# Performance work log

Measured on AMD Instinct MI355X. Metric: run time of the kernel, lower is better.

## Reference

```python
import jax, jax.numpy as jnp
import numpy as np

H = 256  # hidden_size
B = 8192  # batch
S = 1024  # seq_length


def setup_inputs() -> dict:
    key = jax.random.key(0)
    ks = jax.random.split(key, 12)
    lim_g = 1.0 / np.sqrt(1 + H)  # torch Linear default init bound, fan_in = 1+H
    lim_o = 1.0 / np.sqrt(H)
    def lin(k, out_dim, in_dim, lim):
        kw, kb = jax.random.split(k)
        W = jax.random.uniform(kw, (out_dim, in_dim), jnp.float32, -lim, lim)
        b = jax.random.uniform(kb, (out_dim,), jnp.float32, -lim, lim)
        return W, b
    Wf, bf = lin(ks[0], H, 1 + H, lim_g)
    Wi, bi = lin(ks[1], H, 1 + H, lim_g)
    Wc, bc = lin(ks[2], H, 1 + H, lim_g)
    Wo, bo = lin(ks[3], H, 1 + H, lim_g)
    Wout, bout = lin(ks[4], 1, H, lim_o)
    x = jax.random.normal(ks[5], (B, S), jnp.float32)
    return {"x": x, "Wf": Wf, "bf": bf, "Wi": Wi, "bi": bi,
            "Wc": Wc, "bc": bc, "Wo": Wo, "bo": bo,
            "Wout": Wout, "bout": bout}


def reference(x, Wf, bf, Wi, bi, Wc, bc, Wo, bo, Wout, bout):
    B_, S_ = x.shape
    H_ = Wf.shape[0]
    # Fuse the four gate linears into one GEMM per step (same math):
    Wall = jnp.concatenate([Wf, Wi, Wc, Wo], axis=0)      # [4H, 1+H]
    ball = jnp.concatenate([bf, bi, bc, bo], axis=0)      # [4H]

    def step(carry, xt):
        h, c = carry                                       # [B,H], [B,H]
        conc = jnp.concatenate([xt[:, None], h], axis=1)   # [B, 1+H]
        g = conc @ Wall.T + ball                           # [B, 4H]
        f, i, cs, o = jnp.split(g, 4, axis=1)
        c = jax.nn.sigmoid(f) * c + jax.nn.sigmoid(i) * jnp.tanh(cs)
        h = jax.nn.sigmoid(o) * jnp.tanh(c)
        return (h, c), None

    h0 = jnp.zeros((B_, H_), x.dtype)
    c0 = jnp.zeros((B_, H_), x.dtype)
    (h, _), _ = jax.lax.scan(step, (h0, c0), x.T)          # scan over seq axis
    out = h @ Wout.T + bout                                # [B, 1]
    return out.squeeze(-1)                                 # [B]
```

## Files before the change

### kernel.cpp

```cpp
#include <hip/hip_runtime.h>
#include <hip/hip_fp16.h>


typedef _Float16 f16x8 __attribute__((ext_vector_type(8)));
typedef float f32x4 __attribute__((ext_vector_type(4)));
typedef unsigned int u32;
typedef unsigned short u16;

#define WINT_OFF 0u
#define W0B_OFF  524288u
#define FLAG_OFF 528384u
#define PUB_OFF  1048576u

static __device__ __forceinline__ float fast_exp2(float x) {
#if __has_builtin(__builtin_amdgcn_exp2f)
  return __builtin_amdgcn_exp2f(x);
#else
  return exp2f(x);
#endif
}
static __device__ __forceinline__ float fast_rcp(float x) {
#if __has_builtin(__builtin_amdgcn_rcpf)
  return __builtin_amdgcn_rcpf(x);
#else
  return 1.0f / x;
#endif
}
static __device__ __forceinline__ u16 f16b(float f) {
  union { _Float16 h; u16 u; } cv; cv.h = (_Float16)f; return cv.u;
}
static __device__ __forceinline__ float h2f(u16 u) {
  union { u16 u; _Float16 h; } cv; cv.u = u; return (float)cv.h;
}
static __device__ __forceinline__ u16* pub_base(u16* pub, int set, int par,
                                                int pid, int half) {
  return pub + ((size_t)(((set * 2 + par) * 128 + pid) * 2 + half) << 12);
}

__global__ void lstm_prep(const float* __restrict__ Wf, const float* __restrict__ Wi,
                          const float* __restrict__ Wc, const float* __restrict__ Wo,
                          const float* __restrict__ bf_, const float* __restrict__ bi_,
                          const float* __restrict__ bc_, const float* __restrict__ bo_,
                          u16* __restrict__ Wint, u32* __restrict__ w0b) {
  int n = blockIdx.x;
  int k = threadIdx.x;
  int g = n >> 8, j = n & 255;
  const float* Ws = (g == 0) ? Wf : (g == 1) ? Wi : (g == 2) ? Wc : Wo;
  const float scale = (g == 2) ? 2.88539008f : 1.44269504f;
  Wint[n * 256 + k] = f16b(Ws[j * 257 + 1 + k] * scale);
  if (k == 0) {
    const float* bs = (g == 0) ? bf_ : (g == 1) ? bi_ : (g == 2) ? bc_ : bo_;
    w0b[n] = (u32)f16b(Ws[j * 257] * scale) | ((u32)f16b(bs[j] * scale) << 16);
  }
}

__global__ void lstm_zero(uint4* __restrict__ pub4, uint4* __restrict__ flags4,
                          float* __restrict__ out, const float* __restrict__ bout) {
  int idx = blockIdx.x * 256 + threadIdx.x;
  uint4 z = uint4{0, 0, 0, 0};
  if (idx < 131072) pub4[idx] = z;
  else if (idx < 262144) pub4[idx + 131072] = z;
  else if (idx < 264192) flags4[idx - 262144] = z;
  else { int o = idx - 264192; if (o < 8192) out[o] = bout[0]; }
}

__global__ __launch_bounds__(512, 2) void lstm_main(
    const u16* __restrict__ Wint, const u32* __restrict__ w0b,
    const float* __restrict__ x, const float* __restrict__ Wout,
    float* __restrict__ out, u16* __restrict__ pub, int* __restrict__ flags) {

  __shared__ __align__(16) u16 stg[2][2][4096];

  const int tid  = threadIdx.x;
  const int wv   = tid >> 6;
  const int lane = tid & 63;
  const int l15  = lane & 15;
  const int quad = lane >> 4;
  const int B    = blockIdx.x;
  const int mi   = (B >> 3) & 1;
  const int peer = B ^ 8;
  const int pid  = (B & 7) | ((B >> 4) << 3);
  const int rows0 = pid * 64;

  f16x8 wfrag[4][8];
#pragma unroll
  for (int g = 0; g < 4; ++g)
#pragma unroll
    for (int hm = 0; hm < 2; ++hm)
#pragma unroll
      for (int ktl = 0; ktl < 4; ++ktl) {
        int kbase = (hm == 0 ? mi : 1 - mi) * 128 + ktl * 32;
        wfrag[g][hm * 4 + ktl] = *(const f16x8*)(Wint +
            (size_t)(g * 256 + mi * 128 + wv * 16 + l15) * 256 + kbase + quad * 8);
      }
  float w0f[4][4], bsf[4][4];
#pragma unroll
  for (int g = 0; g < 4; ++g) {
    uint4 wv4 = *(const uint4*)(w0b + g * 256 + mi * 128 + wv * 16 + quad * 4);
    u32 pka[4] = {wv4.x, wv4.y, wv4.z, wv4.w};
#pragma unroll
    for (int r = 0; r < 4; ++r) {
      w0f[g][r] = h2f((u16)pka[r]);
      bsf[g][r] = h2f((u16)(pka[r] >> 16));
    }
  }

#pragma unroll
  for (int i = 0; i < 4; ++i) ((uint4*)stg)[tid + i * 512] = uint4{0, 0, 0, 0};

  float cst[2][2][4];
#pragma unroll
  for (int s = 0; s < 2; ++s)
#pragma unroll
    for (int bt = 0; bt < 2; ++bt)
#pragma unroll
      for (int r = 0; r < 4; ++r) cst[s][bt][r] = 0.0f;

  const float* xq = x + (size_t)rows0 * 1024;
  float xcur[2][2];
#pragma unroll
  for (int s = 0; s < 2; ++s)
#pragma unroll
    for (int bt = 0; bt < 2; ++bt)
      xcur[s][bt] = xq[(size_t)(s * 32 + bt * 16 + l15) * 1024];

  int* const myflag = flags + B * 32;
  int* const pfl    = flags + peer * 32;

  __syncthreads();

#pragma unroll 1
  for (int t = 0; t < 1024; ++t) {
#pragma unroll
    for (int s = 0; s < 2; ++s) {
      const int tn = (s == 0) ? t : t + 1;

      int fv = 0;
      if (tn < 1024)
        fv = __hip_atomic_load(pfl + (s ^ 1) * 16, __ATOMIC_RELAXED,
                               __HIP_MEMORY_SCOPE_AGENT);

      f32x4 acc[4][2];
#pragma unroll
      for (int g = 0; g < 4; ++g)
#pragma unroll
        for (int r = 0; r < 4; ++r) {
          acc[g][0][r] = xcur[s][0] * w0f[g][r] + bsf[g][r];
          acc[g][1][r] = xcur[s][1] * w0f[g][r] + bsf[g][r];
        }
#pragma unroll
      for (int bt = 0; bt < 2; ++bt)
        xcur[s][bt] = xq[(size_t)(s * 32 + bt * 16 + l15) * 1024 + ((t + 1) & 1023)];

#pragma unroll
      for (int hm = 0; hm < 2; ++hm)
#pragma unroll
        for (int ktl = 0; ktl < 4; ++ktl) {
          f16x8 bb[2];
#pragma unroll
          for (int bt = 0; bt < 2; ++bt) {
            int b = bt * 16 + l15;
            int cp = (ktl * 4 + quad) ^ (b & 15);
            bb[bt] = *(const f16x8*)(&stg[s][hm][0] + b * 128 + cp * 8);
          }
#pragma unroll
          for (int g = 0; g < 4; ++g)
#pragma unroll
            for (int bt = 0; bt < 2; ++bt)
              acc[g][bt] = __builtin_amdgcn_mfma_f32_16x16x32_f16(
                  wfrag[g][hm * 4 + ktl], bb[bt], acc[g][bt], 0, 0, 0);
        }

      if (tn < 1024) {
        while (fv < tn) {
          __builtin_amdgcn_s_sleep(1);
          fv = __hip_atomic_load(pfl + (s ^ 1) * 16, __ATOMIC_RELAXED,
                                 __HIP_MEMORY_SCOPE_AGENT);
        }
        const u16* srcO = pub_base(pub, s ^ 1, tn & 1, pid, mi);
        const u16* srcP = pub_base(pub, s ^ 1, tn & 1, pid, 1 - mi);
        __builtin_amdgcn_global_load_lds(
            (const __attribute__((address_space(1))) u32*)(srcO + wv * 512 + lane * 8),
            (__attribute__((address_space(3))) u32*)(&stg[s ^ 1][0][wv * 512]), 16, 0, 0);
        __builtin_amdgcn_global_load_lds(
            (const __attribute__((address_space(1))) u32*)(srcP + wv * 512 + lane * 8),
            (__attribute__((address_space(3))) u32*)(&stg[s ^ 1][1][wv * 512]), 16, 0, 0);
      }

      u16* pb = pub_base(pub, s, (t + 1) & 1, pid, mi);
#pragma unroll
      for (int bt = 0; bt < 2; ++bt) {
        int b = bt * 16 + l15;
        u32 lo, hi;
        {
          float h0, h1, h2, h3;
#pragma unroll
          for (int r = 0; r < 4; ++r) {
            float fg = acc[0][bt][r], ig = acc[1][bt][r];
            float cg = acc[2][bt][r], og = acc[3][bt][r];
            float Ef = fast_exp2(-fg);
            float Ei = fast_exp2(-ig);
            float C  = fast_exp2(cg);
            float X  = 1.0f + Ef;
            float Y  = (1.0f + Ei) * (C + 1.0f);
            float num = cst[s][bt][r] * Y + (C - 1.0f) * X;
            float c_  = num * fast_rcp(X * Y);
            cst[s][bt][r] = c_;
            float cc = fminf(fmaxf(c_, -40.0f), 40.0f);
            float T  = fast_exp2(2.88539008f * cc);
            float Eo = fast_exp2(-og);
            float hv = (T - 1.0f) * fast_rcp((1.0f + Eo) * (T + 1.0f));
            if (r == 0) h0 = hv; else if (r == 1) h1 = hv;
            else if (r == 2) h2 = hv; else h3 = hv;
          }
          lo = (u32)f16b(h0) | ((u32)f16b(h1) << 16);
          hi = (u32)f16b(h2) | ((u32)f16b(h3) << 16);
        }
        int c16 = wv * 2 + (quad >> 1);
        int cp  = c16 ^ (b & 15);
        *(uint2*)(pb + b * 128 + cp * 8 + (quad & 1) * 4) = uint2{lo, hi};
      }

      __syncthreads();
      if (tid == 0)
        __hip_atomic_store(myflag + s * 16, t + 1, __ATOMIC_RELAXED,
                           __HIP_MEMORY_SCOPE_AGENT);
    }
  }

  if (tid < 64) {
    int s = tid >> 5, b = tid & 31;
    const u16* pbase = pub_base(pub, s, 0, pid, mi);
    float a = 0.0f;
#pragma unroll
    for (int c = 0; c < 16; ++c) {
      f16x8 hv = *(const f16x8*)(pbase + b * 128 + ((c ^ (b & 15)) * 8));
#pragma unroll
      for (int e = 0; e < 8; ++e) a += (float)hv[e] * Wout[mi * 128 + c * 8 + e];
    }
    atomicAdd(&out[rows0 + s * 32 + b], a);
  }
}

extern "C" void kernel_launch(void* const* d_in, const int* in_sizes, int n_in,
                              void* d_out, int out_size, void* d_ws, size_t ws_size,
                              hipStream_t stream) {
  const float* x    = (const float*)d_in[0];
  const float* Wf   = (const float*)d_in[1];
  const float* bf_  = (const float*)d_in[2];
  const float* Wi   = (const float*)d_in[3];
  const float* bi_  = (const float*)d_in[4];
  const float* Wc   = (const float*)d_in[5];
  const float* bc_  = (const float*)d_in[6];
  const float* Wo   = (const float*)d_in[7];
  const float* bo_  = (const float*)d_in[8];
  const float* Wout = (const float*)d_in[9];
  const float* bout = (const float*)d_in[10];

  u16* Wint  = (u16*)((char*)d_ws + WINT_OFF);
  u32* w0b   = (u32*)((char*)d_ws + W0B_OFF);
  int* flags = (int*)((char*)d_ws + FLAG_OFF);
  u16* pub   = (u16*)((char*)d_ws + PUB_OFF);

  lstm_prep<<<1024, 256, 0, stream>>>(Wf, Wi, Wc, Wo, bf_, bi_, bc_, bo_, Wint, w0b);
  lstm_zero<<<1064, 256, 0, stream>>>((uint4*)pub, (uint4*)flags, (float*)d_out, bout);
  lstm_main<<<256, 512, 0, stream>>>(Wint, w0b, x, Wout, (float*)d_out, pub, flags);
}
```

Measured before the change: 4.963 ms.

## Keep own-half hidden state in LDS and overlap peer wait with local MFMAs

Each block now writes its own half of the new hidden state straight into a double-buffered LDS slot as well as to global memory. It no longer reloads that half from global with global_load_lds. The MFMA loop is split so the own-half product is computed before the peer flag is polled, and the peer-half product runs after. This hides part of the cross-block flag latency and halves the global-to-LDS traffic per step, at the cost of doubling the LDS staging buffer, which may reduce occupancy headroom.

```diff
diff --git a/kernel.cpp b/kernel.cpp
--- a/kernel.cpp
+++ b/kernel.cpp
@@ -69,7 +69,7 @@
     const float* __restrict__ x, const float* __restrict__ Wout,
     float* __restrict__ out, u16* __restrict__ pub, int* __restrict__ flags) {
 
-  __shared__ __align__(16) u16 stg[2][2][4096];
+  __shared__ __align__(16) u16 stg[2][2][2][4096];
 
   const int tid  = threadIdx.x;
   const int wv   = tid >> 6;
@@ -106,7 +106,7 @@
   }
 
 #pragma unroll
-  for (int i = 0; i < 4; ++i) ((uint4*)stg)[tid + i * 512] = uint4{0, 0, 0, 0};
+  for (int i = 0; i < 8; ++i) ((uint4*)stg)[tid + i * 512] = uint4{0, 0, 0, 0};
 
   float cst[2][2][4];
 #pragma unroll
@@ -135,41 +135,56 @@
     for (int s = 0; s < 2; ++s) {
       const int tn = (s == 0) ? t : t + 1;
 
-      int fv = 0;
+      f32x4 acc[4][2];
+#pragma unroll
+      for (int g = 0; g < 4; ++g)
+#pragma unroll
+        for (int r = 0; r < 4; ++r) {
+          acc[g][0][r] = xcur[s][0] * w0f[g][r] + bsf[g][r];
+          acc[g][1][r] = xcur[s][1] * w0f[g][r] + bsf[g][r];
+        }
+#pragma unroll
+      for (int bt = 0; bt < 2; ++bt)
+        xcur[s][bt] = xq[(size_t)(s * 32 + bt * 16 + l15) * 1024 + ((t + 1) & 1023)];
+
+#pragma unroll
+      for (int ktl = 0; ktl < 4; ++ktl) {
+        f16x8 bb[2];
+#pragma unroll
+        for (int bt = 0; bt < 2; ++bt) {
+          int b = bt * 16 + l15;
+          int cp = (ktl * 4 + quad) ^ (b & 15);
+          bb[bt] = *(const f16x8*)(&stg[s][t & 1][0][0] + b * 128 + cp * 8);
+        }
+#pragma unroll
+        for (int g = 0; g < 4; ++g)
+#pragma unroll
+          for (int bt = 0; bt < 2; ++bt)
+            acc[g][bt] = __builtin_amdgcn_mfma_f32_16x16x32_f16(
+                wfrag[g][ktl], bb[bt], acc[g][bt], 0, 0, 0);
+      }
+
+      int fv = 0x7fffffff;
       if (tn < 1024)
         fv = __hip_atomic_load(pfl + (s ^ 1) * 16, __ATOMIC_RELAXED,
                                __HIP_MEMORY_SCOPE_AGENT);
 
-      f32x4 acc[4][2];
-#pragma unroll
-      for (int g = 0; g < 4; ++g)
-#pragma unroll
-        for (int r = 0; r < 4; ++r) {
-          acc[g][0][r] = xcur[s][0] * w0f[g][r] + bsf[g][r];
-          acc[g][1][r] = xcur[s][1] * w0f[g][r] + bsf[g][r];
-        }
-#pragma unroll
-      for (int bt = 0; bt < 2; ++bt)
-        xcur[s][bt] = xq[(size_t)(s * 32 + bt * 16 + l15) * 1024 + ((t + 1) & 1023)];
-
-#pragma unroll
-      for (int hm = 0; hm < 2; ++hm)
-#pragma unroll
-        for (int ktl = 0; ktl < 4; ++ktl) {
-          f16x8 bb[2];
-#pragma unroll
-          for (int bt = 0; bt < 2; ++bt) {
-            int b = bt * 16 + l15;
-            int cp = (ktl * 4 + quad) ^ (b & 15);
-            bb[bt] = *(const f16x8*)(&stg[s][hm][0] + b * 128 + cp * 8);
-          }
-#pragma unroll
-          for (int g = 0; g < 4; ++g)
-#pragma unroll
-            for (int bt = 0; bt < 2; ++bt)
-              acc[g][bt] = __builtin_amdgcn_mfma_f32_16x16x32_f16(
-                  wfrag[g][hm * 4 + ktl], bb[bt], acc[g][bt], 0, 0, 0);
-        }
+#pragma unroll
+      for (int ktl = 0; ktl < 4; ++ktl) {
+        f16x8 bb[2];
+#pragma unroll
+        for (int bt = 0; bt < 2; ++bt) {
+          int b = bt * 16 + l15;
+          int cp = (ktl * 4 + quad) ^ (b & 15);
+          bb[bt] = *(const f16x8*)(&stg[s][t & 1][1][0] + b * 128 + cp * 8);
+        }
+#pragma unroll
+        for (int g = 0; g < 4; ++g)
+#pragma unroll
+          for (int bt = 0; bt < 2; ++bt)
+            acc[g][bt] = __builtin_amdgcn_mfma_f32_16x16x32_f16(
+                wfrag[g][4 + ktl], bb[bt], acc[g][bt], 0, 0, 0);
+      }
 
       if (tn < 1024) {
         while (fv < tn) {
@@ -177,17 +192,15 @@
           fv = __hip_atomic_load(pfl + (s ^ 1) * 16, __ATOMIC_RELAXED,
                                  __HIP_MEMORY_SCOPE_AGENT);
         }
-        const u16* srcO = pub_base(pub, s ^ 1, tn & 1, pid, mi);
         const u16* srcP = pub_base(pub, s ^ 1, tn & 1, pid, 1 - mi);
         __builtin_amdgcn_global_load_lds(
-            (const __attribute__((address_space(1))) u32*)(srcO + wv * 512 + lane * 8),
-            (__attribute__((address_space(3))) u32*)(&stg[s ^ 1][0][wv * 512]), 16, 0, 0);
-        __builtin_amdgcn_global_load_lds(
             (const __attribute__((address_space(1))) u32*)(srcP + wv * 512 + lane * 8),
-            (__attribute__((address_space(3))) u32*)(&stg[s ^ 1][1][wv * 512]), 16, 0, 0);
+            (__attribute__((address_space(3))) u32*)(&stg[s ^ 1][tn & 1][1][wv * 512]),
+            16, 0, 0);
       }
 
       u16* pb = pub_base(pub, s, (t + 1) & 1, pid, mi);
+      u16* lb = &stg[s][(t + 1) & 1][0][0];
 #pragma unroll
       for (int bt = 0; bt < 2; ++bt) {
         int b = bt * 16 + l15;
@@ -217,8 +230,9 @@
           hi = (u32)f16b(h2) | ((u32)f16b(h3) << 16);
         }
         int c16 = wv * 2 + (quad >> 1);
-        int cp  = c16 ^ (b & 15);
-        *(uint2*)(pb + b * 128 + cp * 8 + (quad & 1) * 4) = uint2{lo, hi};
+        int off = b * 128 + (c16 ^ (b & 15)) * 8 + (quad & 1) * 4;
+        *(uint2*)(lb + off) = uint2{lo, hi};
+        *(uint2*)(pb + off) = uint2{lo, hi};
       }
 
       __syncthreads();
```

New measurement: 4.840 ms. -2.5%, faster.
